# Kernel optimization log

Measured on AMD Instinct MI355X. Metric: run time of the kernel, lower is better.

The kernel has to match this reference:

```python
import jax, jax.numpy as jnp
import numpy as np

B, H, W = 16, 16, 16
L = 32          # in_capsules
O = 32          # out_capsules
P = 16          # p_size
PD = 4          # p_dim = sqrt(p_size)
ETA = 1.0


def setup_inputs() -> dict:
    key = jax.random.key(0)
    k1, k2, k3 = jax.random.split(key, 3)
    # [B, H, W, L*(P+1)]: first L*P channels are poses, last L are activations in [0,1]
    input_tensor = jax.random.uniform(k1, (B, H, W, L * (P + 1)), dtype=jnp.float32)
    # transform weights: [L, O, 4, 4] (kernel_size=1, shared over spatial positions)
    weights = jax.random.normal(k2, (L, O, PD, PD), dtype=jnp.float32) / np.sqrt(PD)
    activation_bias = jax.random.uniform(k3, (O,), dtype=jnp.float32)
    return {"input_tensor": input_tensor, "weights": weights,
            "activation_bias": activation_bias}


def reference(input_tensor, weights, activation_bias):
    Bs, Hh, Ww, _ = input_tensor.shape
    M = Hh * Ww
    # split poses / activations
    poses = input_tensor[..., : L * P].reshape(Bs, M, L, PD, PD)   # [B, M, L, 4, 4]
    acts = input_tensor[..., L * P:].reshape(Bs, M * L)            # [B, N]
    # votes[b, (m,l), o] = pose[b,m,l] @ W[l,o]  (shared transform, repeated over M)
    votes = jnp.einsum('bmlij,lojk->bmloik', poses, weights)
    votes = votes.reshape(Bs, M * L, O, P)                         # [B, N, O, 16]
    # weight votes by input activations and group per output capsule
    Y = (acts[:, :, None, None] * votes).transpose(0, 2, 1, 3)     # [B, O, N, 16]
    # top-1 right singular vector via gram matrix eigendecomposition (detached)
    gram = jnp.einsum('bonp,bonq->bopq', Y, Y)                     # [B, O, 16, 16]
    _, V = jnp.linalg.eigh(jax.lax.stop_gradient(gram))            # ascending eigvals
    pose_out = V[..., -1]                                          # [B, O, 16]
    # agreement: ||Y u||^2 / ||Y||_F^2
    yu = jnp.einsum('bonp,bop->bon', Y, pose_out)                  # [B, O, N]
    ratio = (yu ** 2).sum(-1) / (Y ** 2).sum((-1, -2))             # [B, O]
    act_out = jax.nn.sigmoid(ETA * (ratio - activation_bias))      # [B, O]
    return act_out, pose_out
```

## Files before the change

### kernel.cpp

```cpp
#include <hip/hip_runtime.h>

#define B_ 16
#define L_ 32
#define O_ 32
#define M_ 256
#define CH_ 544
#define WS2_STRIDE 320


__device__ __forceinline__ float rl(float v, int lane) {
  return __int_as_float(__builtin_amdgcn_readlane(__float_as_int(v), lane));
}

__device__ __forceinline__ float sum16_rl(float v) {
  float s = rl(v, 0);
#pragma unroll
  for (int j = 1; j < 16; j++) s += rl(v, j);
  return s;
}

__device__ __forceinline__ float frcp(float x) { return __builtin_amdgcn_rcpf(x); }
__device__ __forceinline__ float frsq(float x) { return __builtin_amdgcn_rsqf(x); }


__device__ __forceinline__ float slapy2f(float x, float y) {
  float xa = fabsf(x), ya = fabsf(y);
  float w = fmaxf(xa, ya), z = fminf(xa, ya);
  float q = z * frcp(w);
  float res = w * sqrtf(1.f + q * q);
  return (z == 0.f) ? w : res;
}

__device__ __forceinline__ void slartgf(float f, float g, float* c, float* s, float* r) {
  float t = f * f + g * g;
  float inv = frsq(t);
  float d = t * inv;
  float cg_ = fabsf(f) * inv;
  float rg = copysignf(d, f);
  float sg = g * copysignf(inv, f);
  bool g0 = (g == 0.f), f0 = (f == 0.f);
  *c = g0 ? 1.f : (f0 ? 0.f : cg_);
  *s = g0 ? 0.f : (f0 ? copysignf(1.f, g) : sg);
  *r = g0 ? f : (f0 ? fabsf(g) : rg);
}

__device__ __noinline__ float4 slaev2f(float a, float b, float c) {
  float sm = a + c, df = a - c;
  float adf = fabsf(df);
  float tb = b + b;
  float ab = fabsf(tb);
  float acmx, acmn;
  if (fabsf(a) > fabsf(c)) { acmx = a; acmn = c; } else { acmx = c; acmn = a; }
  float rt;
  if (adf > ab) { float q = ab / adf; rt = adf * sqrtf(1.f + q * q); }
  else if (adf < ab) { float q = adf / ab; rt = ab * sqrtf(1.f + q * q); }
  else rt = ab * sqrtf(2.f);
  float rt1, rt2;
  int sgn1;
  if (sm < 0.f) { rt1 = 0.5f * (sm - rt); sgn1 = -1; rt2 = (acmx / rt1) * acmn - (b / rt1) * b; }
  else if (sm > 0.f) { rt1 = 0.5f * (sm + rt); sgn1 = 1; rt2 = (acmx / rt1) * acmn - (b / rt1) * b; }
  else { rt1 = 0.5f * rt; rt2 = -0.5f * rt; sgn1 = 1; }
  float cs; int sgn2;
  if (df >= 0.f) { cs = df + rt; sgn2 = 1; } else { cs = df - rt; sgn2 = -1; }
  float acs = fabsf(cs), c1, s1;
  if (acs > ab) { float ct = -tb / cs; s1 = 1.f / sqrtf(1.f + ct * ct); c1 = ct * s1; }
  else if (ab == 0.f) { c1 = 1.f; s1 = 0.f; }
  else { float tn = -cs / tb; c1 = 1.f / sqrtf(1.f + tn * tn); s1 = tn * c1; }
  if (sgn1 == sgn2) { float tn = c1; c1 = -s1; s1 = tn; }
  return make_float4(rt1, rt2, c1, s1);
}

__global__ __launch_bounds__(256) void moments_kernel(const float* __restrict__ in,
                                                      float* __restrict__ Tmom) {
  int bl = blockIdx.x;
  int b = bl >> 5, l = bl & 31;
  int t = threadIdx.x;
  int w = t >> 6, lane = t & 63;
  __shared__ __align__(16) float ut[4][16][68];
  __shared__ float red[4][16][16];
  const float* base = in + (size_t)b * (M_ * CH_);
  const float* row = base + (size_t)(w * 64 + lane) * CH_ + l * 16;
  float4 p0 = *(const float4*)(row + 0);
  float4 p1 = *(const float4*)(row + 4);
  float4 p2 = *(const float4*)(row + 8);
  float4 p3 = *(const float4*)(row + 12);
  float a = row[512 - l * 16 + l];
  float (*u)[68] = ut[w];
  u[0][lane] = a * p0.x;  u[1][lane] = a * p0.y;  u[2][lane] = a * p0.z;  u[3][lane] = a * p0.w;
  u[4][lane] = a * p1.x;  u[5][lane] = a * p1.y;  u[6][lane] = a * p1.z;  u[7][lane] = a * p1.w;
  u[8][lane] = a * p2.x;  u[9][lane] = a * p2.y;  u[10][lane] = a * p2.z; u[11][lane] = a * p2.w;
  u[12][lane] = a * p3.x; u[13][lane] = a * p3.y; u[14][lane] = a * p3.z; u[15][lane] = a * p3.w;
  asm volatile("" ::: "memory");
  int c = lane & 15, r0 = lane >> 4;
  float acc0 = 0.f, acc1 = 0.f, acc2 = 0.f, acc3 = 0.f;
#pragma unroll
  for (int m4 = 0; m4 < 64; m4 += 4) {
    float4 cv = *(const float4*)&u[c][m4];
    float4 a0 = *(const float4*)&u[r0][m4];
    float4 a1 = *(const float4*)&u[r0 + 4][m4];
    float4 a2 = *(const float4*)&u[r0 + 8][m4];
    float4 a3 = *(const float4*)&u[r0 + 12][m4];
    acc0 += a0.x * cv.x + a0.y * cv.y + a0.z * cv.z + a0.w * cv.w;
    acc1 += a1.x * cv.x + a1.y * cv.y + a1.z * cv.z + a1.w * cv.w;
    acc2 += a2.x * cv.x + a2.y * cv.y + a2.z * cv.z + a2.w * cv.w;
    acc3 += a3.x * cv.x + a3.y * cv.y + a3.z * cv.z + a3.w * cv.w;
  }
  red[w][r0][c] = acc0;
  red[w][r0 + 4][c] = acc1;
  red[w][r0 + 8][c] = acc2;
  red[w][r0 + 12][c] = acc3;
  __syncthreads();
  int rr_ = t >> 4, cc_ = t & 15;
  float s = (red[0][rr_][cc_] + red[1][rr_][cc_]) + (red[2][rr_][cc_] + red[3][rr_][cc_]);
  Tmom[bl * 256 + t] = s;
}

__global__ __launch_bounds__(64) void gram_sytd2_kernel(const float* __restrict__ Tmom,
                                                        const float* __restrict__ Wt,
                                                        float* __restrict__ ws2) {
  int bo = blockIdx.x;
  int b = bo >> 5, o = bo & 31;
  int lane = threadIdx.x;

  __shared__ __align__(16) float4 Wall4[128];
  __shared__ __align__(16) float4 Tsh4[4 * 18];
  __shared__ float A[16][17];

  const float4* Wt4 = (const float4*)Wt;
#pragma unroll
  for (int k = 0; k < 2; k++) {
    int idx = lane + 64 * k;
    int l = idx >> 2, part = idx & 3;
    Wall4[idx] = Wt4[(l * 32 + o) * 4 + part];
  }
  asm volatile("" ::: "memory");

  int p = lane >> 2;
  int i_ = p >> 2, k_ = p & 3;
  int i2 = lane & 3;
  float gx = 0.f, gy = 0.f, gz = 0.f, gw = 0.f;
  const float4* T4 = (const float4*)(Tmom + (size_t)(b * 32) * 256);
  const float* WallF = (const float*)Wall4;
  float4 t0 = T4[0 * 64 + lane], t1 = T4[1 * 64 + lane];
  float4 t2 = T4[2 * 64 + lane], t3 = T4[3 * 64 + lane];
  for (int l = 0; l < 32; l++) {
    Tsh4[(lane >> 4) * 18 + (lane & 15)] = t0;
    asm volatile("" ::: "memory");
    t0 = t1; t1 = t2; t2 = t3;
    if (l + 4 < 32) t3 = T4[(l + 4) * 64 + lane];
    float4 wq0 = Wall4[l * 4 + 0], wq1 = Wall4[l * 4 + 1];
    float4 wq2 = Wall4[l * 4 + 2], wq3 = Wall4[l * 4 + 3];
#pragma unroll
    for (int jj = 0; jj < 4; jj++) {
      float4 trow = Tsh4[i_ * 18 + jj * 4 + i2];
      float ux = trow.x * wq0.x + trow.y * wq1.x + trow.z * wq2.x + trow.w * wq3.x;
      float uy = trow.x * wq0.y + trow.y * wq1.y + trow.z * wq2.y + trow.w * wq3.y;
      float uz = trow.x * wq0.z + trow.y * wq1.z + trow.z * wq2.z + trow.w * wq3.z;
      float uw = trow.x * wq0.w + trow.y * wq1.w + trow.z * wq2.w + trow.w * wq3.w;
      float wk = WallF[l * 16 + jj * 4 + k_];
      gx += wk * ux; gy += wk * uy; gz += wk * uz; gw += wk * uw;
    }
    asm volatile("" ::: "memory");
  }
  {
    int q0 = i2 * 4;
    A[p][q0 + 0] = gx; A[p][q0 + 1] = gy; A[p][q0 + 2] = gz; A[p][q0 + 3] = gw;
  }
  asm volatile("" ::: "memory");

  int c16 = lane & 15;
  float a[16];
#pragma unroll
  for (int r = 0; r < 16; r++) a[r] = A[r][c16];

  float trace;
  {
    float diag = 0.f;
#pragma unroll
    for (int r = 0; r < 16; r++) if (c16 == r) diag = a[r];
    trace = sum16_rl((lane < 16) ? diag : 0.f);
  }

  float dreg = 0.f, ereg = 0.f, taureg = 0.f;
  float hv[14];
#pragma unroll
  for (int i = 0; i < 15; i++) {
    float cn = 0.f;
#pragma unroll
    for (int r = i + 2; r < 16; r++) cn += a[r] * a[r];
    float xn2 = rl(cn, i);
    float alpha = rl(a[i + 1], i);
    float taui = 0.f;
    float vc = 0.f;
    if (xn2 == 0.f) {
      if (lane == i) ereg = alpha;
    } else {
      float xnorm = sqrtf(xn2);
      float beta = -copysignf(slapy2f(alpha, xnorm), alpha);
      taui = (beta - alpha) / beta;
      float rs = 1.f / (alpha - beta);
      if (lane == i) ereg = beta;
      vc = (lane == i + 1) ? 1.f : ((lane >= i + 2 && lane < 16) ? a[i] * rs : 0.f);
      float vb[16];
#pragma unroll
      for (int r = i + 1; r < 16; r++) vb[r] = rl(vc, r);
      float acc = 0.f;
#pragma unroll
      for (int r = i + 1; r < 16; r++) acc += a[r] * vb[r];
      float wc = (lane >= i + 1 && lane < 16) ? taui * acc : 0.f;
      float wb[16];
#pragma unroll
      for (int r = i + 1; r < 16; r++) wb[r] = rl(wc, r);
      float dot = 0.f;
#pragma unroll
      for (int r = i + 1; r < 16; r++) dot += vb[r] * wb[r];
      float alph2 = -0.5f * taui * dot;
      wc += alph2 * vc;
#pragma unroll
      for (int r = i + 1; r < 16; r++) wb[r] += alph2 * vb[r];
#pragma unroll
      for (int r = i + 1; r < 16; r++) a[r] -= vb[r] * wc + wb[r] * vc;
    }
    if (i < 14) hv[i] = vc;
    if (lane == i) taureg = taui;
  }
#pragma unroll
  for (int r = 0; r < 16; r++) if (c16 == r) dreg = a[r];
  if (lane >= 16) dreg = 0.f;

  float z[16];
#pragma unroll
  for (int r = 0; r < 16; r++) z[r] = (lane == r) ? 1.f : 0.f;
#pragma unroll
  for (int i = 13; i >= 0; i--) {
    float taui = rl(taureg, i);
    if (taui != 0.f) {
      float vbq[16];
      float s = 0.f;
#pragma unroll
      for (int r = i + 1; r < 16; r++) { vbq[r] = rl(hv[i], r); s += vbq[r] * z[r]; }
      s *= taui;
#pragma unroll
      for (int r = i + 1; r < 16; r++) z[r] -= vbq[r] * s;
    }
  }

  float* basep = ws2 + (size_t)bo * WS2_STRIDE;
  if (lane < 16) {
    float4* dst = (float4*)(basep + lane * 16);
    dst[0] = make_float4(z[0], z[1], z[2], z[3]);
    dst[1] = make_float4(z[4], z[5], z[6], z[7]);
    dst[2] = make_float4(z[8], z[9], z[10], z[11]);
    dst[3] = make_float4(z[12], z[13], z[14], z[15]);
    basep[256 + lane] = dreg;
  }
  if (lane < 15) basep[272 + lane] = ereg;
  if (lane == 0) basep[288] = trace;
}

__global__ __launch_bounds__(64) void steqr_kernel(const float* __restrict__ ws2,
                                                   const float* __restrict__ bias,
                                                   float* __restrict__ out) {
  int bo = blockIdx.x;
  int o = bo & 31;
  int lane = threadIdx.x;
  int c16 = lane & 15;
  const float* basep = ws2 + (size_t)bo * WS2_STRIDE;

  float biasv = bias[o];
  float trace = basep[288];
  float zz[16];
#pragma unroll
  for (int k = 0; k < 16; k++) zz[k] = (lane < 16) ? basep[k * 16 + c16] : 0.f;
  float dreg = (lane < 16) ? basep[256 + lane] : 0.f;
  float ereg = (lane < 15) ? basep[272 + lane] : 0.f;
  float dsh = (lane < 15) ? basep[256 + lane + 1] : 0.f;

  const float eps = 5.9604645e-08f;
  const float eps2 = eps * eps;
  const float safmin = 1.17549435e-38f;
  int l1 = 0, jtot = 0;
  const int nmaxit = 480;

  while (l1 < 16) {
    if (l1 > 0) { if (lane == l1 - 1) ereg = 0.f; }
    bool co = (lane < 15) &&
              ((ereg == 0.f) ||
               (fabsf(ereg) <= __builtin_amdgcn_sqrtf(fabsf(dreg)) *
                                   __builtin_amdgcn_sqrtf(fabsf(dsh)) * eps));
    unsigned long long bm = __ballot(co) & ~((1ull << l1) - 1ull);
    int m = bm ? (__ffsll(bm) - 1) : 15;
    if (m < 15) { if (lane == m) ereg = 0.f; }
    int l = l1, lend = m;
    l1 = m + 1;
    if (lend == l) continue;
    {
      float dl = rl(dreg, l), dle = rl(dreg, lend);
      if (fabsf(dle) < fabsf(dl)) { int tq = l; l = lend; lend = tq; }
    }

    if (lend > l) {
      for (;;) {
        bool cj = (lane < 15) && ((ereg * ereg) <= eps2 * fabsf(dreg) * fabsf(dsh) + safmin);
        int mq;
        if (l != lend) {
          unsigned long long bb2 = __ballot(cj) & ((1ull << lend) - 1ull) & ~((1ull << l) - 1ull);
          mq = bb2 ? (__ffsll(bb2) - 1) : lend;
        } else mq = lend;
        if (mq < lend) { if (lane == mq) ereg = 0.f; }
        if (mq == l) { l++; if (l <= lend) continue; break; }
        if (mq == l + 1) {
          float4 ev = slaev2f(rl(dreg, l), rl(ereg, l), rl(dreg, l + 1));
          float rt1 = ev.x, rt2 = ev.y, cc = ev.z, ss = ev.w;
#pragma unroll
          for (int k = 0; k < 15; k++) if (k == l) {
            float z1 = zz[k + 1], z0v = zz[k];
            zz[k + 1] = cc * z1 - ss * z0v;
            zz[k] = ss * z1 + cc * z0v;
          }
          if (lane == l) { dreg = rt1; ereg = 0.f; dsh = rt2; }
          if (lane == l + 1) dreg = rt2;
          if (lane == l - 1) dsh = rt1;
          l += 2; if (l <= lend) continue; break;
        }
        if (jtot == nmaxit) break;
        jtot++;
        float d0 = dreg, e0 = ereg;
        float dArr[16], eArr[15];
#pragma unroll
        for (int r = 0; r < 16; r++) dArr[r] = rl(d0, r);
#pragma unroll
        for (int r = 0; r < 15; r++) eArr[r] = rl(e0, r);
        float pp = rl(d0, l);
        float e_lv = rl(e0, l);
        float gg = (rl(d0, l + 1) - pp) * 0.5f * frcp(e_lv);
        float rr = slapy2f(gg, 1.f);
        gg = rl(d0, mq) - pp + e_lv * frcp(gg + copysignf(rr, gg));
        float ss_ = 1.f, cc_ = 1.f;
        pp = 0.f;
#pragma unroll
        for (int i = 14; i >= 0; i--) {
          if (i <= mq - 1 && i >= l) {
            float e_i = eArr[i], d_i = dArr[i], d_i1 = dArr[i + 1];
            float ff = ss_ * e_i, bb = cc_ * e_i;
            slartgf(gg, ff, &cc_, &ss_, &rr);
            if (i != mq - 1) { if (lane == i + 1) ereg = rr; }
            gg = d_i1 - pp;
            rr = (d_i - gg) * ss_ + 2.f * cc_ * bb;
            pp = ss_ * rr;
            float dnew = gg + pp;
            if (lane == i + 1) dreg = dnew;
            if (lane == i) dsh = dnew;
            gg = cc_ * rr - bb;
            float z1 = zz[i + 1], z0v = zz[i];
            zz[i + 1] = cc_ * z1 + ss_ * z0v;
            zz[i] = -ss_ * z1 + cc_ * z0v;
          }
        }
        float dlv = rl(d0, l) - pp;
        if (lane == l) { dreg = dlv; ereg = gg; }
        if (lane == l - 1) dsh = dlv;
      }
    } else {
      for (;;) {
        bool cj = (lane < 15) && ((ereg * ereg) <= eps2 * fabsf(dreg) * fabsf(dsh) + safmin);
        int mq;
        if (l != lend) {
          unsigned long long bb2 = __ballot(cj) & ((1ull << l) - 1ull) & ~((1ull << lend) - 1ull);
          mq = bb2 ? (63 - __clzll(bb2) + 1) : lend;
        } else mq = lend;
        if (mq > lend) { if (lane == mq - 1) ereg = 0.f; }
        if (mq == l) { l--; if (l >= lend) continue; break; }
        if (mq == l - 1) {
          float4 ev = slaev2f(rl(dreg, l - 1), rl(ereg, l - 1), rl(dreg, l));
          float rt1 = ev.x, rt2 = ev.y, cc = ev.z, ss = ev.w;
#pragma unroll
          for (int k = 0; k < 15; k++) if (k == l - 1) {
            float z1 = zz[k + 1], z0v = zz[k];
            zz[k + 1] = cc * z1 - ss * z0v;
            zz[k] = ss * z1 + cc * z0v;
          }
          if (lane == l - 1) { dreg = rt1; ereg = 0.f; dsh = rt2; }
          if (lane == l) dreg = rt2;
          if (lane == l - 2) dsh = rt1;
          l -= 2; if (l >= lend) continue; break;
        }
        if (jtot == nmaxit) break;
        jtot++;
        float d0 = dreg, e0 = ereg;
        float dArr[16], eArr[15];
#pragma unroll
        for (int r = 0; r < 16; r++) dArr[r] = rl(d0, r);
#pragma unroll
        for (int r = 0; r < 15; r++) eArr[r] = rl(e0, r);
        float pp = rl(d0, l);
        float e_lm1 = rl(e0, l - 1);
        float gg = (rl(d0, l - 1) - pp) * 0.5f * frcp(e_lm1);
        float rr = slapy2f(gg, 1.f);
        gg = rl(d0, mq) - pp + e_lm1 * frcp(gg + copysignf(rr, gg));
        float ss_ = 1.f, cc_ = 1.f;
        pp = 0.f;
#pragma unroll
        for (int i = 0; i <= 14; i++) {
          if (i >= mq && i <= l - 1) {
            float e_i = eArr[i], d_i = dArr[i], d_i1 = dArr[i + 1];
            float ff = ss_ * e_i, bb = cc_ * e_i;
            slartgf(gg, ff, &cc_, &ss_, &rr);
            if (i != mq) { if (lane == i - 1) ereg = rr; }
            gg = d_i - pp;
            rr = (d_i1 - gg) * ss_ + 2.f * cc_ * bb;
            pp = ss_ * rr;
            float dnew = gg + pp;
            if (lane == i) dreg = dnew;
            if (lane == i - 1) dsh = dnew;
            gg = cc_ * rr - bb;
            float z1 = zz[i + 1], z0v = zz[i];
            zz[i + 1] = cc_ * z1 - ss_ * z0v;
            zz[i] = ss_ * z1 + cc_ * z0v;
          }
        }
        float dlv = rl(d0, l) - pp;
        if (lane == l) dreg = dlv;
        if (lane == l - 1) { ereg = gg; dsh = dlv; }
      }
    }
  }

  float mx = rl(dreg, 0);
  int k = 0;
#pragma unroll
  for (int j = 1; j < 16; j++) {
    float dj = rl(dreg, j);
    if (dj > mx) { mx = dj; k = j; }
  }
  float ratio = mx / trace;
  float act = 1.f / (1.f + expf(-(ratio - biasv)));
  float zk = zz[0];
#pragma unroll
  for (int j = 1; j < 16; j++) zk = (k == j) ? zz[j] : zk;
  if (lane < 16) out[512 + bo * 16 + lane] = zk;
  if (lane == 0) out[bo] = act;
}

extern "C" void kernel_launch(void* const* d_in, const int* in_sizes, int n_in,
                              void* d_out, int out_size, void* d_ws, size_t ws_size,
                              hipStream_t stream) {
  const float* in = (const float*)d_in[0];
  const float* w = (const float*)d_in[1];
  const float* bias = (const float*)d_in[2];
  float* out = (float*)d_out;
  float* Tmom = (float*)d_ws;
  float* ws2 = (float*)d_ws + 512 * 256;

  moments_kernel<<<B_ * L_, 256, 0, stream>>>(in, Tmom);
  gram_sytd2_kernel<<<B_ * O_, 64, 0, stream>>>(Tmom, w, ws2);
  steqr_kernel<<<B_ * O_, 64, 0, stream>>>(ws2, bias, out);
}
```

Before: 135.0 us.

## Fuse tridiagonalization and QL eigen-solve kernels, coalesce moment loads

Merges the gram/tridiagonalization kernel and the implicit QL eigen-solver kernel into one. The Householder Q matrix now passes through shared memory, and the diagonal and off-diagonal stay in registers instead of round-tripping through global workspace. This removes one kernel launch and a global write/read per (b,o). Separately, the moments kernel now loads poses so that four lanes cover one row's 16 floats. This coalesces the reads, and activations are shared via LDS. The fused kernel may use more registers, which could lower occupancy.

Result: no change. 134.4 us (-0.5%).

```diff
diff --git a/kernel.cpp b/kernel.cpp
--- a/kernel.cpp
+++ b/kernel.cpp
@@ -5,7 +5,6 @@
 #define O_ 32
 #define M_ 256
 #define CH_ 544
-#define WS2_STRIDE 320
 
 
 __device__ __forceinline__ float rl(float v, int lane) {
@@ -77,21 +76,44 @@
   int t = threadIdx.x;
   int w = t >> 6, lane = t & 63;
   __shared__ __align__(16) float ut[4][16][68];
+  __shared__ float ash[4][64];
   __shared__ float red[4][16][16];
   const float* base = in + (size_t)b * (M_ * CH_);
-  const float* row = base + (size_t)(w * 64 + lane) * CH_ + l * 16;
-  float4 p0 = *(const float4*)(row + 0);
-  float4 p1 = *(const float4*)(row + 4);
-  float4 p2 = *(const float4*)(row + 8);
-  float4 p3 = *(const float4*)(row + 12);
-  float a = row[512 - l * 16 + l];
-  float (*u)[68] = ut[w];
-  u[0][lane] = a * p0.x;  u[1][lane] = a * p0.y;  u[2][lane] = a * p0.z;  u[3][lane] = a * p0.w;
-  u[4][lane] = a * p1.x;  u[5][lane] = a * p1.y;  u[6][lane] = a * p1.z;  u[7][lane] = a * p1.w;
-  u[8][lane] = a * p2.x;  u[9][lane] = a * p2.y;  u[10][lane] = a * p2.z; u[11][lane] = a * p2.w;
-  u[12][lane] = a * p3.x; u[13][lane] = a * p3.y; u[14][lane] = a * p3.z; u[15][lane] = a * p3.w;
+  int mrow = lane >> 2, q = lane & 3;
+  int row0 = w * 64;
+  float4 p0 = *(const float4*)(base + (size_t)(row0 + 0 * 16 + mrow) * CH_ + l * 16 + q * 4);
+  float4 p1 = *(const float4*)(base + (size_t)(row0 + 1 * 16 + mrow) * CH_ + l * 16 + q * 4);
+  float4 p2 = *(const float4*)(base + (size_t)(row0 + 2 * 16 + mrow) * CH_ + l * 16 + q * 4);
+  float4 p3 = *(const float4*)(base + (size_t)(row0 + 3 * 16 + mrow) * CH_ + l * 16 + q * 4);
+  float a = base[(size_t)(row0 + lane) * CH_ + 512 + l];
+  ash[w][lane] = a;
+  asm volatile("" ::: "memory");
+  {
+    float aa0 = ash[w][0 * 16 + mrow];
+    float aa1 = ash[w][1 * 16 + mrow];
+    float aa2 = ash[w][2 * 16 + mrow];
+    float aa3 = ash[w][3 * 16 + mrow];
+    float (*u)[68] = ut[w];
+    u[q * 4 + 0][0 * 16 + mrow] = aa0 * p0.x;
+    u[q * 4 + 1][0 * 16 + mrow] = aa0 * p0.y;
+    u[q * 4 + 2][0 * 16 + mrow] = aa0 * p0.z;
+    u[q * 4 + 3][0 * 16 + mrow] = aa0 * p0.w;
+    u[q * 4 + 0][1 * 16 + mrow] = aa1 * p1.x;
+    u[q * 4 + 1][1 * 16 + mrow] = aa1 * p1.y;
+    u[q * 4 + 2][1 * 16 + mrow] = aa1 * p1.z;
+    u[q * 4 + 3][1 * 16 + mrow] = aa1 * p1.w;
+    u[q * 4 + 0][2 * 16 + mrow] = aa2 * p2.x;
+    u[q * 4 + 1][2 * 16 + mrow] = aa2 * p2.y;
+    u[q * 4 + 2][2 * 16 + mrow] = aa2 * p2.z;
+    u[q * 4 + 3][2 * 16 + mrow] = aa2 * p2.w;
+    u[q * 4 + 0][3 * 16 + mrow] = aa3 * p3.x;
+    u[q * 4 + 1][3 * 16 + mrow] = aa3 * p3.y;
+    u[q * 4 + 2][3 * 16 + mrow] = aa3 * p3.z;
+    u[q * 4 + 3][3 * 16 + mrow] = aa3 * p3.w;
+  }
   asm volatile("" ::: "memory");
   int c = lane & 15, r0 = lane >> 4;
+  float (*u)[68] = ut[w];
   float acc0 = 0.f, acc1 = 0.f, acc2 = 0.f, acc3 = 0.f;
 #pragma unroll
   for (int m4 = 0; m4 < 64; m4 += 4) {
@@ -115,9 +137,10 @@
   Tmom[bl * 256 + t] = s;
 }
 
-__global__ __launch_bounds__(64) void gram_sytd2_kernel(const float* __restrict__ Tmom,
-                                                        const float* __restrict__ Wt,
-                                                        float* __restrict__ ws2) {
+__global__ __launch_bounds__(64) void gram_eig_kernel(const float* __restrict__ Tmom,
+                                                      const float* __restrict__ Wt,
+                                                      const float* __restrict__ bias,
+                                                      float* __restrict__ out) {
   int bo = blockIdx.x;
   int b = bo >> 5, o = bo & 31;
   int lane = threadIdx.x;
@@ -125,6 +148,9 @@
   __shared__ __align__(16) float4 Wall4[128];
   __shared__ __align__(16) float4 Tsh4[4 * 18];
   __shared__ float A[16][17];
+  __shared__ __align__(16) float Zt[16][16];
+
+  float biasv = bias[o];
 
   const float4* Wt4 = (const float4*)Wt;
 #pragma unroll
@@ -244,43 +270,25 @@
       for (int r = i + 1; r < 16; r++) z[r] -= vbq[r] * s;
     }
   }
-
-  float* basep = ws2 + (size_t)bo * WS2_STRIDE;
   if (lane < 16) {
-    float4* dst = (float4*)(basep + lane * 16);
-    dst[0] = make_float4(z[0], z[1], z[2], z[3]);
-    dst[1] = make_float4(z[4], z[5], z[6], z[7]);
-    dst[2] = make_float4(z[8], z[9], z[10], z[11]);
-    dst[3] = make_float4(z[12], z[13], z[14], z[15]);
-    basep[256 + lane] = dreg;
-  }
-  if (lane < 15) basep[272 + lane] = ereg;
-  if (lane == 0) basep[288] = trace;
-}
-
-__global__ __launch_bounds__(64) void steqr_kernel(const float* __restrict__ ws2,
-                                                   const float* __restrict__ bias,
-                                                   float* __restrict__ out) {
-  int bo = blockIdx.x;
-  int o = bo & 31;
-  int lane = threadIdx.x;
-  int c16 = lane & 15;
-  const float* basep = ws2 + (size_t)bo * WS2_STRIDE;
-
-  float biasv = bias[o];
-  float trace = basep[288];
+    float4* zt4 = (float4*)&Zt[lane][0];
+    zt4[0] = make_float4(z[0], z[1], z[2], z[3]);
+    zt4[1] = make_float4(z[4], z[5], z[6], z[7]);
+    zt4[2] = make_float4(z[8], z[9], z[10], z[11]);
+    zt4[3] = make_float4(z[12], z[13], z[14], z[15]);
+  }
+  asm volatile("" ::: "memory");
+
   float zz[16];
 #pragma unroll
-  for (int k = 0; k < 16; k++) zz[k] = (lane < 16) ? basep[k * 16 + c16] : 0.f;
-  float dreg = (lane < 16) ? basep[256 + lane] : 0.f;
-  float ereg = (lane < 15) ? basep[272 + lane] : 0.f;
-  float dsh = (lane < 15) ? basep[256 + lane + 1] : 0.f;
+  for (int k2 = 0; k2 < 16; k2++) zz[k2] = (lane < 16) ? Zt[k2][c16] : 0.f;
 
   const float eps = 5.9604645e-08f;
   const float eps2 = eps * eps;
   const float safmin = 1.17549435e-38f;
   int l1 = 0, jtot = 0;
   const int nmaxit = 480;
+  float dsh = __shfl(dreg, (lane + 1) & 63, 64);
 
   while (l1 < 16) {
     if (l1 > 0) { if (lane == l1 - 1) ereg = 0.f; }
@@ -450,9 +458,7 @@
   const float* bias = (const float*)d_in[2];
   float* out = (float*)d_out;
   float* Tmom = (float*)d_ws;
-  float* ws2 = (float*)d_ws + 512 * 256;
 
   moments_kernel<<<B_ * L_, 256, 0, stream>>>(in, Tmom);
-  gram_sytd2_kernel<<<B_ * O_, 64, 0, stream>>>(Tmom, w, ws2);
-  steqr_kernel<<<B_ * O_, 64, 0, stream>>>(ws2, bias, out);
-}
+  gram_eig_kernel<<<B_ * O_, 64, 0, stream>>>(Tmom, w, bias, out);
+}
```
